# Performance work log

Measured on AMD Instinct MI355X. Metric: run time of the kernel, lower is better.

The kernel has to match this reference:

```python
import jax, jax.numpy as jnp
import numpy as np

B, K, N, D, H, NNEG, NTOP = 8, 8, 128, 256, 128, 64, 64
UNARY_SCALES = (1.0, 1.0, 1.0)  # one scale per tree level, tree_height = log2(K) = 3


def setup_inputs():
    key = jax.random.key(0)
    ks = jax.random.split(key, 8)
    s = 0.05
    return {
        'pos_fea': jax.random.normal(ks[0], (B, K, N, D), jnp.float32),
        'neg_fea': jax.random.normal(ks[1], (B * K, NNEG, D), jnp.float32),
        'pos_classes': jax.random.randint(ks[2], (B, K, N), 0, 20),
        'target_class': jax.random.randint(ks[3], (B,), 0, 20),
        'Wp1': jax.random.normal(ks[4], (2 * D, H), jnp.float32) * s,
        'bp1': jnp.zeros((H,), jnp.float32),
        'Wp2': jax.random.normal(ks[5], (H, 1), jnp.float32) * s,
        'bp2': jnp.zeros((1,), jnp.float32),
        'Wu1': jax.random.normal(ks[6], (2 * D, H), jnp.float32) * s,
        'bu1': jnp.zeros((H,), jnp.float32),
        'Wu2': jax.random.normal(ks[7], (H, 1), jnp.float32) * s,
        'bu2': jnp.zeros((1,), jnp.float32),
    }


def _relation(f0, f1, W1, b1, W2, b2):
    # RelationModule: Dense(H, relu) -> Dense(1) applied to concat([f0_m, f1_n])
    # for every cross pair; concat-Dense is split into two GEMMs. -> [Bn, M0, M1]
    d = f0.shape[-1]
    h0 = jnp.einsum('bmd,dh->bmh', f0, W1[:d])
    h1 = jnp.einsum('bnd,dh->bnh', f1, W1[d:])
    h = jax.nn.relu(h0[:, :, None, :] + h1[:, None, :, :] + b1)
    return jnp.einsum('bmnh,h->bmn', h, W2[:, 0]) + b2[0]


def _bg(t, idx):
    # batched_gather along axis 1: t [Bn, P, ...], idx [Bn, T]
    ie = idx.reshape(idx.shape + (1,) * (t.ndim - 2))
    ie = jnp.broadcast_to(ie, idx.shape + t.shape[2:])
    return jnp.take_along_axis(t, ie, axis=1)


def _rep(fea, sub):
    # subproblem representative feature: fea [Bn,S,N,D], sub [Bn,M,S] -> [Bn,M,D]
    idx = jnp.swapaxes(sub, 1, 2)[..., None]              # [Bn,S,M,1]
    idx = jnp.broadcast_to(idx, idx.shape[:-1] + (fea.shape[-1],))
    return jnp.take_along_axis(fea, idx, axis=2).mean(axis=1)


def _tree(pos_fea, neg_fea, Wp1, bp1, Wp2, bp2, Wu1, bu1, Wu2, bu2):
    pos_flat = pos_fea.reshape(B * K, N, D)
    # UnaryModule: mean relation score of each positive proposal vs the negative bag
    ue = _relation(pos_flat, neg_fea, Wu1, bu1, Wu2, bu2).mean(-1)   # [B*K, N]
    sub = jnp.broadcast_to(jnp.arange(N, dtype=jnp.int32)[None, :, None], (B * K, N, 1))
    pe = jnp.zeros_like(ue)
    tree_height = int(np.log2(K))
    best = None
    for i in range(tree_height):
        S = 2 ** i                      # subproblem size per branch at this level
        Bn = sub.shape[0] // 2
        M = sub.shape[1]
        sub2 = sub.reshape(Bn, 2, M, S)  # [::2] / [1::2] split of adjacent rows
        sub0, sub1 = sub2[:, 0], sub2[:, 1]
        pe2 = pe.reshape(Bn, 2, M)
        ue2 = ue.reshape(Bn, 2, M)
        fea = pos_flat.reshape(Bn, 2, S, N, D)
        rep0 = _rep(fea[:, 0], sub0)
        rep1 = _rep(fea[:, 1], sub1)
        # PairwiseCrossSimilarity: scores for all cross pairs of candidates
        scores = _relation(rep0, rep1, Wp1, bp1, Wp2, bp2).reshape(Bn, M * M)
        p0 = jnp.repeat(jnp.arange(M), M)
        p1 = jnp.tile(jnp.arange(M), M)
        pe = pe2[:, 0][:, p0] + pe2[:, 1][:, p1] - scores
        ue = ue2[:, 0][:, p0] + ue2[:, 1][:, p1]
        total = pe + UNARY_SCALES[i] * ue
        sub = jnp.concatenate([sub0[:, p0], sub1[:, p1]], axis=-1)  # [Bn, M*M, 2S]
        topk = 1 if i == tree_height - 1 else min(M * M, NTOP)
        _, inds = jax.lax.top_k(-total, topk)
        sub = _bg(sub, inds)
        ue = jnp.take_along_axis(ue, inds, axis=1)
        pe = jnp.take_along_axis(pe, inds, axis=1)
        best = jnp.take_along_axis(total, inds, axis=1)
    return sub, best


def reference(pos_fea, neg_fea, pos_classes, target_class,
              Wp1, bp1, Wp2, bp2, Wu1, bu1, Wu2, bu2):
    sub, _ = _tree(pos_fea, neg_fea, Wp1, bp1, Wp2, bp2, Wu1, bu1, Wu2, bu2)
    is_target = (pos_classes == target_class[:, None, None]).astype(jnp.float32)
    return sub[:, 0], is_target  # selected proposal per image [B,K], [B,K,N]
```

## Files before the change

### kernel.cpp

```cpp
#include <hip/hip_runtime.h>
#include <stdint.h>

#define B_ 8
#define K_ 8
#define N_ 128
#define D_ 256
#define H_ 128
#define NNEG_ 64

typedef unsigned long long u64;

__device__ __forceinline__ u64 shfl_xor_u64(u64 v, int m) {
    int lo = __shfl_xor((int)(unsigned)v, m, 64);
    int hi = __shfl_xor((int)(unsigned)(v >> 32), m, 64);
    return ((u64)(unsigned)hi << 32) | (unsigned)lo;
}
__device__ __forceinline__ u64 bitonic_merge64(u64 m, int lane) {
#pragma unroll
    for (int j = 32; j > 0; j >>= 1) {
        u64 o = shfl_xor_u64(m, j);
        bool keepMin = ((lane & j) == 0);
        bool lt = m < o;
        m = (keepMin == lt) ? m : o;
    }
    return m;
}
__device__ __forceinline__ unsigned sortable(float f) {
    unsigned u = __float_as_uint(f);
    return (u & 0x80000000u) ? ~u : (u | 0x80000000u);
}
__device__ __forceinline__ float unsortable(unsigned u) {
    return __uint_as_float((u & 0x80000000u) ? (u & 0x7FFFFFFFu) : ~u);
}
__device__ __forceinline__ void sort128_wave0(u64* cand, int cc, int lane) {
    u64 v0 = (lane < cc) ? cand[lane] : ~0ull;
    u64 v1 = (64 + lane < cc) ? cand[64 + lane] : ~0ull;
#pragma unroll
    for (int k = 2; k <= 64; k <<= 1) {
        bool d0 = ((lane & k) == 0);
        bool d1 = (k == 64) ? false : d0;
#pragma unroll
        for (int j = k >> 1; j > 0; j >>= 1) {
            u64 o0 = shfl_xor_u64(v0, j);
            bool km0 = (((lane & j) == 0) == d0);
            v0 = (km0 == (v0 < o0)) ? v0 : o0;
            u64 o1 = shfl_xor_u64(v1, j);
            bool km1 = (((lane & j) == 0) == d1);
            v1 = (km1 == (v1 < o1)) ? v1 : o1;
        }
    }
    if (v0 > v1) { u64 tmp = v0; v0 = v1; v1 = tmp; }
#pragma unroll
    for (int j = 32; j > 0; j >>= 1) {
        bool km = ((lane & j) == 0);
        u64 o0 = shfl_xor_u64(v0, j);
        v0 = (km == (v0 < o0)) ? v0 : o0;
        u64 o1 = shfl_xor_u64(v1, j);
        v1 = (km == (v1 < o1)) ? v1 : o1;
    }
    cand[lane] = v0; cand[64 + lane] = v1;
}

__global__ __launch_bounds__(256) void g1_gemm(
    const float* __restrict__ pos, const float* __restrict__ neg,
    const float* __restrict__ Wu1, const float* __restrict__ Wp1,
    const int* __restrict__ pos_classes, const int* __restrict__ target_class,
    float* __restrict__ HU0, float* __restrict__ HU1n,
    float* __restrict__ HP0, float* __restrict__ HP1,
    float* __restrict__ outp) {
    int bid = blockIdx.x;
    int t = threadIdx.x;
    if (bid >= 448) {
        int base = (bid - 448) * 2048 + t * 8;
#pragma unroll
        for (int q = 0; q < 8; ++q) {
            int idx = base + q;
            outp[64 + idx] = (pos_classes[idx] == target_class[idx >> 10]) ? 1.0f : 0.0f;
        }
        return;
    }
    const float* A; const float* W; float* OUT; int rb;
    if (bid < 128)      { A = pos; W = Wu1;           OUT = HU0;  rb = bid * 64; }
    else if (bid < 192) { A = neg; W = Wu1 + D_ * H_; OUT = HU1n; rb = (bid - 128) * 64; }
    else if (bid < 320) { A = pos; W = Wp1;           OUT = HP0;  rb = (bid - 192) * 64; }
    else                { A = pos; W = Wp1 + D_ * H_; OUT = HP1;  rb = (bid - 320) * 64; }

    __shared__ float AsT[16][68];
    __shared__ float Bs[16][140];
    int tx = t & 15, ty = t >> 4;
    int pb0 = tx * 8 + 4 * (tx >> 2);
    float acc[4][8];
#pragma unroll
    for (int i = 0; i < 4; ++i)
#pragma unroll
        for (int j = 0; j < 8; ++j) acc[i][j] = 0.f;

    for (int k0 = 0; k0 < D_; k0 += 16) {
        {
            int row = t >> 2, kq = (t & 3) * 4;
            float4 av = *(const float4*)&A[(size_t)(rb + row) * D_ + k0 + kq];
            AsT[kq + 0][row] = av.x;
            AsT[kq + 1][row] = av.y;
            AsT[kq + 2][row] = av.z;
            AsT[kq + 3][row] = av.w;
        }
#pragma unroll
        for (int i = t; i < 512; i += 256) {
            int kr = i >> 5, c4 = (i & 31) * 4;
            int ph = c4 + 4 * (c4 >> 5);
            *(float4*)&Bs[kr][ph] = *(const float4*)&W[(size_t)(k0 + kr) * H_ + c4];
        }
        __syncthreads();
#pragma unroll
        for (int kk = 0; kk < 16; ++kk) {
            float4 av = *(const float4*)&AsT[kk][ty * 4];
            float4 b0 = *(const float4*)&Bs[kk][pb0];
            float4 b1 = *(const float4*)&Bs[kk][pb0 + 4];
#pragma unroll
            for (int i = 0; i < 4; ++i) {
                float a = (&av.x)[i];
                acc[i][0] += a * b0.x;
                acc[i][1] += a * b0.y;
                acc[i][2] += a * b0.z;
                acc[i][3] += a * b0.w;
                acc[i][4] += a * b1.x;
                acc[i][5] += a * b1.y;
                acc[i][6] += a * b1.z;
                acc[i][7] += a * b1.w;
            }
        }
        __syncthreads();
    }
#pragma unroll
    for (int i = 0; i < 4; ++i) {
        int row = rb + ty * 4 + i;
        float4 o0 = {acc[i][0], acc[i][1], acc[i][2], acc[i][3]};
        float4 o1 = {acc[i][4], acc[i][5], acc[i][6], acc[i][7]};
        *(float4*)&OUT[(size_t)row * H_ + tx * 8] = o0;
        *(float4*)&OUT[(size_t)row * H_ + tx * 8 + 4] = o1;
    }
}

__global__ __launch_bounds__(256) void g2_ue_sc0(
    const float* __restrict__ HU0, const float* __restrict__ HU1n,
    const float* __restrict__ bu1, const float* __restrict__ Wu2,
    const float* __restrict__ bu2v,
    const float* __restrict__ HP0, const float* __restrict__ HP1,
    const float* __restrict__ bp1, const float* __restrict__ Wp2,
    const float* __restrict__ bp2,
    float* __restrict__ t0, float* __restrict__ sc0) {
    __shared__ float Ls[32][132];
    __shared__ float Rs[64][132];
    __shared__ float wsv[128];
    __shared__ float red[32][33];

    int bid = blockIdx.x;
    int t = threadIdx.x;
    bool is_ue = bid < 256;

    if (is_ue) {
        int bk = bid >> 2, mt = bid & 3;
        for (int i = t; i < 64 * 128; i += 256) {
            int n = i >> 7, h = i & 127;
            Rs[n][h] = HU1n[(size_t)(bk * NNEG_ + n) * H_ + h];
        }
        for (int i = t; i < 32 * 128; i += 256) {
            int m = i >> 7, h = i & 127;
            Ls[m][h] = HU0[(size_t)(bk * N_ + mt * 32 + m) * H_ + h] + bu1[h];
        }
        if (t < 128) wsv[t] = Wu2[t];
    } else {
        int bid2 = bid - 256;
        int b = bid2 >> 3, m0t = (bid2 >> 1) & 3, m1t = bid2 & 1;
        const float* Lg = HP0 + (size_t)b * 2 * N_ * H_ + m0t * 32 * H_;
        const float* Rg = HP1 + (size_t)b * 2 * N_ * H_ + N_ * H_ + m1t * 64 * H_;
        for (int i = t; i < 64 * 128; i += 256) {
            int n = i >> 7, h = i & 127;
            Rs[n][h] = Rg[(size_t)n * H_ + h];
        }
        for (int i = t; i < 32 * 128; i += 256) {
            int m = i >> 7, h = i & 127;
            Ls[m][h] = Lg[(size_t)m * H_ + h] + bp1[h];
        }
        if (t < 128) wsv[t] = Wp2[t];
    }
    __syncthreads();

    int tm = t & 7, tn = t >> 3;
    float a00 = 0.f, a01 = 0.f, a10 = 0.f, a11 = 0.f;
    float a20 = 0.f, a21 = 0.f, a30 = 0.f, a31 = 0.f;
#pragma unroll 2
    for (int h = 0; h < 128; h += 4) {
        float4 wv = *(const float4*)&wsv[h];
        float4 r0 = *(const float4*)&Rs[tn * 2][h];
        float4 r1 = *(const float4*)&Rs[tn * 2 + 1][h];
        float4 l0 = *(const float4*)&Ls[tm][h];
        float4 l1 = *(const float4*)&Ls[tm + 8][h];
        float4 l2 = *(const float4*)&Ls[tm + 16][h];
        float4 l3 = *(const float4*)&Ls[tm + 24][h];
#pragma unroll
        for (int c = 0; c < 4; ++c) {
            float w = (&wv.x)[c];
            float b0 = (&r0.x)[c], b1 = (&r1.x)[c];
            float x0 = (&l0.x)[c], x1 = (&l1.x)[c];
            float x2 = (&l2.x)[c], x3 = (&l3.x)[c];
            float v;
            v = x0 + b0; v = v > 0.f ? v : 0.f; a00 += v * w;
            v = x0 + b1; v = v > 0.f ? v : 0.f; a01 += v * w;
            v = x1 + b0; v = v > 0.f ? v : 0.f; a10 += v * w;
            v = x1 + b1; v = v > 0.f ? v : 0.f; a11 += v * w;
            v = x2 + b0; v = v > 0.f ? v : 0.f; a20 += v * w;
            v = x2 + b1; v = v > 0.f ? v : 0.f; a21 += v * w;
            v = x3 + b0; v = v > 0.f ? v : 0.f; a30 += v * w;
            v = x3 + b1; v = v > 0.f ? v : 0.f; a31 += v * w;
        }
    }

    if (is_ue) {
        int bk = bid >> 2, mt = bid & 3;
        red[tm + 0][tn] = a00 + a01;
        red[tm + 8][tn] = a10 + a11;
        red[tm + 16][tn] = a20 + a21;
        red[tm + 24][tn] = a30 + a31;
        __syncthreads();
        if (t < 32) {
            float s = 0.f;
            for (int q = 0; q < 32; ++q) s += red[t][q];
            t0[bk * N_ + mt * 32 + t] = s * (1.0f / NNEG_) + bu2v[0];
        }
    } else {
        int bid2 = bid - 256;
        int b = bid2 >> 3, m0t = (bid2 >> 1) & 3, m1t = bid2 & 1;
        float bp2v = bp2[0];
        float* orow = sc0 + (size_t)b * 16384;
        float accs[4][2] = {{a00, a01}, {a10, a11}, {a20, a21}, {a30, a31}};
#pragma unroll
        for (int i = 0; i < 4; ++i) {
            int m0 = m0t * 32 + tm + 8 * i;
#pragma unroll
            for (int j = 0; j < 2; ++j) {
                int m1 = m1t * 64 + tn * 2 + j;
                orow[m0 * 128 + m1] = accs[i][j] + bp2v;
            }
        }
    }
}

__global__ __launch_bounds__(1024) void g3_top0(const float* __restrict__ sc0,
                                                const float* __restrict__ t0,
                                                float* __restrict__ tA,
                                                int* __restrict__ pA) {
    int r = blockIdx.x;
    int t = threadIdx.x, lane = t & 63;
    __shared__ float tt[256];
    __shared__ unsigned cnt[16][2];
    __shared__ unsigned ccnt;
    __shared__ u64 cand[128];
    if (t < 256) tt[t] = t0[r * 256 + t];
    if (t < 32) cnt[t >> 1][t & 1] = 0u;
    if (t == 0) ccnt = 0u;
    __syncthreads();
    const float* row = sc0 + (size_t)r * 16384;
    unsigned sv[16];
#pragma unroll
    for (int j = 0; j < 16; ++j) {
        int idx = j * 1024 + t;
        float v = (tt[idx >> 7] + tt[128 + (idx & 127)]) - row[idx];
        sv[j] = sortable(v);
    }
    unsigned T = 0u;
#pragma unroll
    for (int it = 0; it < 16; ++it) {
        int p = 30 - 2 * it;
        unsigned C1 = T | (1u << p), C2 = T | (2u << p), C3 = T | (3u << p);
        unsigned c13 = 0u, c2 = 0u;
#pragma unroll
        for (int j = 0; j < 16; ++j) {
            c13 += (sv[j] < C1) ? 1u : 0u;
            c13 += (sv[j] < C3) ? 0x10000u : 0u;
            c2 += (sv[j] < C2) ? 1u : 0u;
        }
#pragma unroll
        for (int off = 32; off > 0; off >>= 1) {
            c13 += (unsigned)__shfl_xor((int)c13, off, 64);
            c2 += (unsigned)__shfl_xor((int)c2, off, 64);
        }
        if (lane == 0) { atomicAdd(&cnt[it][0], c13); atomicAdd(&cnt[it][1], c2); }
        __syncthreads();
        unsigned t13 = cnt[it][0], t2v = cnt[it][1];
        unsigned t1 = t13 & 0xFFFFu, t3 = t13 >> 16;
        unsigned k = (t3 < 64u) ? 3u : (t2v < 64u) ? 2u : (t1 < 64u) ? 1u : 0u;
        T |= (k << p);
    }
#pragma unroll
    for (int j = 0; j < 16; ++j) {
        if (sv[j] <= T) {
            unsigned pos = atomicAdd(&ccnt, 1u);
            if (pos < 128u) {
                int idx = j * 1024 + t;
                cand[pos] = ((u64)sv[j] << 32) | (unsigned)idx;
            }
        }
    }
    __syncthreads();
    if (t < 64) {
        int cc = (int)(ccnt < 128u ? ccnt : 128u);
        sort128_wave0(cand, cc, lane);
        u64 kk = cand[lane];
        int idx = (int)(kk & 0xFFFFFFFFull);
        tA[r * 64 + lane] = unsortable((unsigned)(kk >> 32));
        pA[r * 64 + lane] = ((idx >> 7) << 8) | (idx & 127);
    }
}

__global__ __launch_bounds__(256) void g4a_s1(
    const float* __restrict__ HP0, const float* __restrict__ HP1,
    const float* __restrict__ tA, const int* __restrict__ pA,
    const float* __restrict__ bp1, const float* __restrict__ Wp2,
    const float* __restrict__ bp2, u64* __restrict__ g4top) {
    int bid = blockIdx.x;
    int u = bid >> 1, half = bid & 1;
    int t = threadIdx.x, lane = t & 63, w = t >> 6;
    __shared__ float LsT[128][68];
    __shared__ float RsT[128][36];
    __shared__ float taL[64], taR[64];
    __shared__ int paL[64], paR[64];
    __shared__ float wsv[128];
    __shared__ unsigned cnt[16][2];
    __shared__ unsigned ccnt;
    __shared__ u64 cand[128];
    if (t < 64) { taL[t] = tA[(2 * u) * 64 + t]; paL[t] = pA[(2 * u) * 64 + t]; }
    else if (t < 128) { int e = t - 64; taR[e] = tA[(2 * u + 1) * 64 + e]; paR[e] = pA[(2 * u + 1) * 64 + e]; }
    if (t < 128) wsv[t] = Wp2[t];
    if (t < 32) cnt[t >> 1][t & 1] = 0u;
    if (t == 0) ccnt = 0u;
    float bp2v = bp2[0];
    __syncthreads();
    for (int i = t; i < 64 * 128; i += 256) {
        int m = i >> 7, h = i & 127;
        int pk = paL[m]; int a0 = pk >> 8, a1 = pk & 255;
        float s = HP0[(size_t)(4 * u) * 16384 + a0 * 128 + h]
                + HP0[(size_t)(4 * u + 1) * 16384 + a1 * 128 + h];
        LsT[h][m] = s * 0.5f + bp1[h];
    }
    for (int i = t; i < 32 * 128; i += 256) {
        int n = i >> 7, h = i & 127;
        int ng = half * 32 + n;
        int pk = paR[ng]; int c0 = pk >> 8, c1 = pk & 255;
        float s = HP1[(size_t)(4 * u + 2) * 16384 + c0 * 128 + h]
                + HP1[(size_t)(4 * u + 3) * 16384 + c1 * 128 + h];
        RsT[h][n] = s * 0.5f;
    }
    __syncthreads();
    int qm = w * 4 + (lane >> 4);
    int qn = lane & 15;
    float acc[4][2];
#pragma unroll
    for (int i = 0; i < 4; ++i) { acc[i][0] = 0.f; acc[i][1] = 0.f; }
#pragma unroll 2
    for (int h = 0; h < 128; ++h) {
        float4 lv = *(const float4*)&LsT[h][qm * 4];
        float2 rv = *(const float2*)&RsT[h][qn * 2];
        float wv = wsv[h];
        float v;
        v = lv.x + rv.x; v = v > 0.f ? v : 0.f; acc[0][0] += v * wv;
        v = lv.x + rv.y; v = v > 0.f ? v : 0.f; acc[0][1] += v * wv;
        v = lv.y + rv.x; v = v > 0.f ? v : 0.f; acc[1][0] += v * wv;
        v = lv.y + rv.y; v = v > 0.f ? v : 0.f; acc[1][1] += v * wv;
        v = lv.z + rv.x; v = v > 0.f ? v : 0.f; acc[2][0] += v * wv;
        v = lv.z + rv.y; v = v > 0.f ? v : 0.f; acc[2][1] += v * wv;
        v = lv.w + rv.x; v = v > 0.f ? v : 0.f; acc[3][0] += v * wv;
        v = lv.w + rv.y; v = v > 0.f ? v : 0.f; acc[3][1] += v * wv;
    }
    unsigned sv[8];
#pragma unroll
    for (int mi = 0; mi < 4; ++mi) {
#pragma unroll
        for (int nj = 0; nj < 2; ++nj) {
            int m = qm * 4 + mi;
            int ng = half * 32 + qn * 2 + nj;
            float val = (taL[m] + taR[ng]) - (acc[mi][nj] + bp2v);
            sv[mi * 2 + nj] = sortable(val);
        }
    }
    unsigned T = 0u;
#pragma unroll
    for (int it = 0; it < 16; ++it) {
        int p = 30 - 2 * it;
        unsigned C1 = T | (1u << p), C2 = T | (2u << p), C3 = T | (3u << p);
        unsigned c13 = 0u, c2 = 0u;
#pragma unroll
        for (int j = 0; j < 8; ++j) {
            c13 += (sv[j] < C1) ? 1u : 0u;
            c13 += (sv[j] < C3) ? 0x10000u : 0u;
            c2 += (sv[j] < C2) ? 1u : 0u;
        }
#pragma unroll
        for (int off = 32; off > 0; off >>= 1) {
            c13 += (unsigned)__shfl_xor((int)c13, off, 64);
            c2 += (unsigned)__shfl_xor((int)c2, off, 64);
        }
        if (lane == 0) { atomicAdd(&cnt[it][0], c13); atomicAdd(&cnt[it][1], c2); }
        __syncthreads();
        unsigned t13 = cnt[it][0], t2v = cnt[it][1];
        unsigned t1 = t13 & 0xFFFFu, t3 = t13 >> 16;
        unsigned k = (t3 < 64u) ? 3u : (t2v < 64u) ? 2u : (t1 < 64u) ? 1u : 0u;
        T |= (k << p);
    }
#pragma unroll
    for (int j = 0; j < 8; ++j) {
        if (sv[j] <= T) {
            unsigned pos = atomicAdd(&ccnt, 1u);
            if (pos < 128u) {
                int mi = j >> 1, nj = j & 1;
                int idx = (qm * 4 + mi) * 64 + half * 32 + qn * 2 + nj;
                cand[pos] = ((u64)sv[j] << 32) | (unsigned)idx;
            }
        }
    }
    __syncthreads();
    if (w == 0) {
        int cc = (int)(ccnt < 128u ? ccnt : 128u);
        sort128_wave0(cand, cc, lane);
        g4top[(size_t)bid * 64 + lane] = cand[lane];
    }
}

__global__ __launch_bounds__(256) void g4b_s2(
    const float* __restrict__ HP0, const float* __restrict__ HP1,
    const int* __restrict__ pA, const u64* __restrict__ g4top,
    const float* __restrict__ bp1, const float* __restrict__ Wp2,
    const float* __restrict__ bp2, float* __restrict__ outp) {
    int b = blockIdx.x;
    int t = threadIdx.x, lane = t & 63, w = t >> 6;
    __shared__ float LsT[128][68];
    __shared__ float RsT[128][36];
    __shared__ float tL[64], tR[64];
    __shared__ unsigned subL[64], subR[64];
    __shared__ float wsv[128];
    __shared__ u64 sred[4];
    if (t < 128) wsv[t] = Wp2[t];
    float bp2v = bp2[0];
    if (w < 2) {
        const u64* A = g4top + (size_t)(4 * b + 2 * w) * 64;
        const u64* Bp = g4top + (size_t)(4 * b + 2 * w + 1) * 64;
        u64 x = A[lane], y = Bp[63 - lane];
        u64 m = x < y ? x : y;
        m = bitonic_merge64(m, lane);
        int idx = (int)(m & 0xFFFFFFFFull);
        int p0 = idx >> 6, p1 = idx & 63;
        float val = unsortable((unsigned)(m >> 32));
        int rowL = 4 * b + 2 * w;
        int pkL = pA[rowL * 64 + p0];
        int pkR = pA[(rowL + 1) * 64 + p1];
        unsigned leaves = ((unsigned)pkL << 16) | (unsigned)pkR;
        if (w == 0) { tL[lane] = val; subL[lane] = leaves; }
        else        { tR[lane] = val; subR[lane] = leaves; }
    }
    __syncthreads();
    for (int i = t; i < 64 * 128; i += 256) {
        int m = i >> 7, h = i & 127;
        unsigned s4 = subL[m];
        float s = HP0[(size_t)(8 * b + 0) * 16384 + ((s4 >> 24) & 255u) * 128 + h]
                + HP0[(size_t)(8 * b + 1) * 16384 + ((s4 >> 16) & 255u) * 128 + h]
                + HP0[(size_t)(8 * b + 2) * 16384 + ((s4 >> 8) & 255u) * 128 + h]
                + HP0[(size_t)(8 * b + 3) * 16384 + (s4 & 255u) * 128 + h];
        LsT[h][m] = s * 0.25f + bp1[h];
    }
    u64 best = ~0ull;
    int qm = w * 4 + (lane >> 4);
    int qn = lane & 15;
    for (int half = 0; half < 2; ++half) {
        __syncthreads();
        for (int i = t; i < 32 * 128; i += 256) {
            int n = i >> 7, h = i & 127;
            int ng = half * 32 + n;
            unsigned s4 = subR[ng];
            float s = HP1[(size_t)(8 * b + 4) * 16384 + ((s4 >> 24) & 255u) * 128 + h]
                    + HP1[(size_t)(8 * b + 5) * 16384 + ((s4 >> 16) & 255u) * 128 + h]
                    + HP1[(size_t)(8 * b + 6) * 16384 + ((s4 >> 8) & 255u) * 128 + h]
                    + HP1[(size_t)(8 * b + 7) * 16384 + (s4 & 255u) * 128 + h];
            RsT[h][n] = s * 0.25f;
        }
        __syncthreads();
        float acc[4][2];
#pragma unroll
        for (int i = 0; i < 4; ++i) { acc[i][0] = 0.f; acc[i][1] = 0.f; }
#pragma unroll 2
        for (int h = 0; h < 128; ++h) {
            float4 lv = *(const float4*)&LsT[h][qm * 4];
            float2 rv = *(const float2*)&RsT[h][qn * 2];
            float wv = wsv[h];
            float v;
            v = lv.x + rv.x; v = v > 0.f ? v : 0.f; acc[0][0] += v * wv;
            v = lv.x + rv.y; v = v > 0.f ? v : 0.f; acc[0][1] += v * wv;
            v = lv.y + rv.x; v = v > 0.f ? v : 0.f; acc[1][0] += v * wv;
            v = lv.y + rv.y; v = v > 0.f ? v : 0.f; acc[1][1] += v * wv;
            v = lv.z + rv.x; v = v > 0.f ? v : 0.f; acc[2][0] += v * wv;
            v = lv.z + rv.y; v = v > 0.f ? v : 0.f; acc[2][1] += v * wv;
            v = lv.w + rv.x; v = v > 0.f ? v : 0.f; acc[3][0] += v * wv;
            v = lv.w + rv.y; v = v > 0.f ? v : 0.f; acc[3][1] += v * wv;
        }
#pragma unroll
        for (int mi = 0; mi < 4; ++mi) {
#pragma unroll
            for (int nj = 0; nj < 2; ++nj) {
                int m = qm * 4 + mi;
                int ng = half * 32 + qn * 2 + nj;
                float val = (tL[m] + tR[ng]) - (acc[mi][nj] + bp2v);
                u64 kk = ((u64)sortable(val) << 32) | (unsigned)(m * 64 + ng);
                best = kk < best ? kk : best;
            }
        }
    }
#pragma unroll
    for (int off = 32; off > 0; off >>= 1) {
        u64 o = shfl_xor_u64(best, off);
        best = o < best ? o : best;
    }
    if (lane == 0) sred[w] = best;
    __syncthreads();
    if (t == 0) {
        u64 bb = sred[0];
        for (int p = 1; p < 4; ++p) { u64 o = sred[p]; bb = o < bb ? o : bb; }
        int idx = (int)(bb & 0xFFFFFFFFull);
        unsigned sl = subL[idx >> 6], sr = subR[idx & 63];
        outp[b * 8 + 0] = (float)((sl >> 24) & 255u);
        outp[b * 8 + 1] = (float)((sl >> 16) & 255u);
        outp[b * 8 + 2] = (float)((sl >> 8) & 255u);
        outp[b * 8 + 3] = (float)(sl & 255u);
        outp[b * 8 + 4] = (float)((sr >> 24) & 255u);
        outp[b * 8 + 5] = (float)((sr >> 16) & 255u);
        outp[b * 8 + 6] = (float)((sr >> 8) & 255u);
        outp[b * 8 + 7] = (float)(sr & 255u);
    }
}

extern "C" void kernel_launch(void* const* d_in, const int* in_sizes, int n_in,
                              void* d_out, int out_size, void* d_ws, size_t ws_size,
                              hipStream_t stream) {
    const float* pos = (const float*)d_in[0];
    const float* neg = (const float*)d_in[1];
    const int* pos_classes = (const int*)d_in[2];
    const int* target_class = (const int*)d_in[3];
    const float* Wp1 = (const float*)d_in[4];
    const float* bp1 = (const float*)d_in[5];
    const float* Wp2 = (const float*)d_in[6];
    const float* bp2 = (const float*)d_in[7];
    const float* Wu1 = (const float*)d_in[8];
    const float* bu1 = (const float*)d_in[9];
    const float* Wu2 = (const float*)d_in[10];
    const float* bu2 = (const float*)d_in[11];

    float* wsf = (float*)d_ws;
    float* HU0 = wsf;
    float* HP0 = HU0 + 1048576;
    float* HP1 = HP0 + 1048576;
    float* HU1n = HP1 + 1048576;
    float* t0 = HU1n + 524288;
    float* sc0 = t0 + 8192;
    float* tA = sc0 + 524288;
    int* pA = (int*)(tA + 2048);
    u64* g4top = (u64*)(pA + 2048);
    float* outp = (float*)d_out;

    g1_gemm<<<452, 256, 0, stream>>>(pos, neg, Wu1, Wp1, pos_classes,
                                     target_class, HU0, HU1n, HP0, HP1, outp);
    g2_ue_sc0<<<512, 256, 0, stream>>>(HU0, HU1n, bu1, Wu2, bu2,
                                       HP0, HP1, bp1, Wp2, bp2, t0, sc0);
    g3_top0<<<32, 1024, 0, stream>>>(sc0, t0, tA, pA);
    g4a_s1<<<32, 256, 0, stream>>>(HP0, HP1, tA, pA, bp1, Wp2, bp2, g4top);
    g4b_s2<<<8, 256, 0, stream>>>(HP0, HP1, pA, g4top, bp1, Wp2, bp2, outp);
}
```

Before: 209.1 us.

## Split GEMM blocks into column halves and read weights directly from global

The first GEMM kernel now splits each 64-row tile into two 64-column halves, doubling the block count to raise parallelism across CUs. The weight tile is no longer staged in shared memory; each thread reads its 8 weight columns straight from global memory/cache, while the A tile is staged with a larger 64-deep k-chunk, halving the number of barriers. Each thread computes a 2x8 output instead of 4x8, which lowers arithmetic intensity per load and relies on cache hits for the repeated weight reads.

```diff
diff --git a/kernel.cpp b/kernel.cpp
--- a/kernel.cpp
+++ b/kernel.cpp
@@ -70,8 +70,8 @@
     float* __restrict__ outp) {
     int bid = blockIdx.x;
     int t = threadIdx.x;
-    if (bid >= 448) {
-        int base = (bid - 448) * 2048 + t * 8;
+    if (bid >= 896) {
+        int base = (bid - 896) * 2048 + t * 8;
 #pragma unroll
         for (int q = 0; q < 8; ++q) {
             int idx = base + q;
@@ -79,45 +79,45 @@
         }
         return;
     }
+    int rt = bid >> 1, half = bid & 1;
     const float* A; const float* W; float* OUT; int rb;
-    if (bid < 128)      { A = pos; W = Wu1;           OUT = HU0;  rb = bid * 64; }
-    else if (bid < 192) { A = neg; W = Wu1 + D_ * H_; OUT = HU1n; rb = (bid - 128) * 64; }
-    else if (bid < 320) { A = pos; W = Wp1;           OUT = HP0;  rb = (bid - 192) * 64; }
-    else                { A = pos; W = Wp1 + D_ * H_; OUT = HP1;  rb = (bid - 320) * 64; }
-
-    __shared__ float AsT[16][68];
-    __shared__ float Bs[16][140];
-    int tx = t & 15, ty = t >> 4;
-    int pb0 = tx * 8 + 4 * (tx >> 2);
-    float acc[4][8];
-#pragma unroll
-    for (int i = 0; i < 4; ++i)
+    if (rt < 128)      { A = pos; W = Wu1;           OUT = HU0;  rb = rt * 64; }
+    else if (rt < 192) { A = neg; W = Wu1 + D_ * H_; OUT = HU1n; rb = (rt - 128) * 64; }
+    else if (rt < 320) { A = pos; W = Wp1;           OUT = HP0;  rb = (rt - 192) * 64; }
+    else               { A = pos; W = Wp1 + D_ * H_; OUT = HP1;  rb = (rt - 320) * 64; }
+    int cb = half * 64;
+
+    __shared__ float AsT[64][66];
+
+    int tx = t & 7;
+    int tyr = t >> 3;
+    const float* Wc = W + cb + tx * 8;
+    float acc[2][8];
+#pragma unroll
+    for (int i = 0; i < 2; ++i)
 #pragma unroll
         for (int j = 0; j < 8; ++j) acc[i][j] = 0.f;
 
-    for (int k0 = 0; k0 < D_; k0 += 16) {
-        {
-            int row = t >> 2, kq = (t & 3) * 4;
+    for (int k0 = 0; k0 < D_; k0 += 64) {
+#pragma unroll
+        for (int q = 0; q < 4; ++q) {
+            int idx = q * 256 + t;
+            int row = idx >> 4, kq = (idx & 15) * 4;
             float4 av = *(const float4*)&A[(size_t)(rb + row) * D_ + k0 + kq];
             AsT[kq + 0][row] = av.x;
             AsT[kq + 1][row] = av.y;
             AsT[kq + 2][row] = av.z;
             AsT[kq + 3][row] = av.w;
         }
-#pragma unroll
-        for (int i = t; i < 512; i += 256) {
-            int kr = i >> 5, c4 = (i & 31) * 4;
-            int ph = c4 + 4 * (c4 >> 5);
-            *(float4*)&Bs[kr][ph] = *(const float4*)&W[(size_t)(k0 + kr) * H_ + c4];
-        }
-        __syncthreads();
-#pragma unroll
-        for (int kk = 0; kk < 16; ++kk) {
-            float4 av = *(const float4*)&AsT[kk][ty * 4];
-            float4 b0 = *(const float4*)&Bs[kk][pb0];
-            float4 b1 = *(const float4*)&Bs[kk][pb0 + 4];
-#pragma unroll
-            for (int i = 0; i < 4; ++i) {
+        __syncthreads();
+#pragma unroll 8
+        for (int kk = 0; kk < 64; ++kk) {
+            float2 av = *(const float2*)&AsT[kk][tyr * 2];
+            const float* wrow = Wc + (size_t)(k0 + kk) * H_;
+            float4 b0 = *(const float4*)&wrow[0];
+            float4 b1 = *(const float4*)&wrow[4];
+#pragma unroll
+            for (int i = 0; i < 2; ++i) {
                 float a = (&av.x)[i];
                 acc[i][0] += a * b0.x;
                 acc[i][1] += a * b0.y;
@@ -132,12 +132,12 @@
         __syncthreads();
     }
 #pragma unroll
-    for (int i = 0; i < 4; ++i) {
-        int row = rb + ty * 4 + i;
+    for (int i = 0; i < 2; ++i) {
+        int row = rb + tyr * 2 + i;
         float4 o0 = {acc[i][0], acc[i][1], acc[i][2], acc[i][3]};
         float4 o1 = {acc[i][4], acc[i][5], acc[i][6], acc[i][7]};
-        *(float4*)&OUT[(size_t)row * H_ + tx * 8] = o0;
-        *(float4*)&OUT[(size_t)row * H_ + tx * 8 + 4] = o1;
+        *(float4*)&OUT[(size_t)row * H_ + cb + tx * 8] = o0;
+        *(float4*)&OUT[(size_t)row * H_ + cb + tx * 8 + 4] = o1;
     }
 }
 
@@ -564,7 +564,7 @@
     u64* g4top = (u64*)(pA + 2048);
     float* outp = (float*)d_out;
 
-    g1_gemm<<<452, 256, 0, stream>>>(pos, neg, Wu1, Wp1, pos_classes,
+    g1_gemm<<<900, 256, 0, stream>>>(pos, neg, Wu1, Wp1, pos_classes,
                                      target_class, HU0, HU1n, HP0, HP1, outp);
     g2_ue_sc0<<<512, 256, 0, stream>>>(HU0, HU1n, bu1, Wu2, bu2,
                                        HP0, HP1, bp1, Wp2, bp2, t0, sc0);
```

Measured after the change: 239.2 us. 14.4% more time.
